# Kernel tuning notes

Measured on AMD Instinct MI355X. Metric: run time of the kernel, lower is better.

The kernel has to match this reference:

```python
import jax, jax.numpy as jnp
import numpy as np

N_HEAD = 8
D_MODEL = 512
D_K = 64
D_V = 64
LN_EPS = 1e-6


def setup_inputs() -> dict:
    key = jax.random.key(0)
    ks = jax.random.split(key, 8)
    B, L = 4, 1024
    inp = {
        "q": jax.random.normal(ks[0], (B, L, D_MODEL), dtype=jnp.float32),
        "k": jax.random.normal(ks[1], (B, L, D_MODEL), dtype=jnp.float32),
        "v": jax.random.normal(ks[2], (B, L, D_MODEL), dtype=jnp.float32),
        "w_qs": jax.random.normal(ks[3], (D_MODEL, N_HEAD * D_K), dtype=jnp.float32) * 0.02,
        "w_ks": jax.random.normal(ks[4], (D_MODEL, N_HEAD * D_K), dtype=jnp.float32) * 0.02,
        "w_vs": jax.random.normal(ks[5], (D_MODEL, N_HEAD * D_V), dtype=jnp.float32) * 0.02,
        "w_sk": jax.random.normal(ks[6], (D_V, N_HEAD * D_V), dtype=jnp.float32) * 0.02,
        "w_fc": jax.random.normal(ks[7], (D_V, D_MODEL), dtype=jnp.float32) * 0.02,
        "ln_gamma": jnp.ones((D_MODEL,), dtype=jnp.float32),
        "ln_beta": jnp.zeros((D_MODEL,), dtype=jnp.float32),
    }
    return inp


def reference(q, k, v, w_qs, w_ks, w_vs, w_sk, w_fc, ln_gamma, ln_beta):
    B, Lq, _ = q.shape
    Lk = k.shape[1]
    temp = jnp.asarray(D_K ** 0.5, q.dtype)
    residual = q

    # QKV projections (bias=False), split heads: [B, H, L, d]
    qh = (q @ w_qs).reshape(B, Lq, N_HEAD, D_K).transpose(0, 2, 1, 3)
    kh = (k @ w_ks).reshape(B, Lk, N_HEAD, D_K).transpose(0, 2, 1, 3)
    vh = (v @ w_vs).reshape(B, Lk, N_HEAD, D_V).transpose(0, 2, 1, 3)

    # scaled dot-product attention (dropout in eval mode = identity)
    attn = jax.nn.softmax(jnp.einsum('bhqd,bhkd->bhqk', qh / temp, kh), axis=-1)
    o = jnp.einsum('bhqk,bhkd->bhqd', attn, vh)  # [B, H, Lq, D_V]

    # SPA: selective parallel attention head gating
    u = o.sum(axis=1)                       # [B, Lq, D_V]
    s = u.mean(axis=1)                      # adaptive avg pool over Lq -> [B, D_V]
    g = jax.nn.softmax((s @ w_sk).reshape(B, N_HEAD, D_V), axis=1)  # softmax over heads
    f = o * g[:, :, None, :]                # gate each head, broadcast over Lq
    qo = f.sum(axis=1)                      # sum heads -> [B, Lq, D_V]

    # fc + residual + LayerNorm (dropout eval = identity)
    out = qo @ w_fc + residual              # [B, Lq, D_MODEL]
    mu = out.mean(axis=-1, keepdims=True)
    var = out.var(axis=-1, keepdims=True)
    out = (out - mu) * jax.lax.rsqrt(var + LN_EPS) * ln_gamma + ln_beta
    return out, attn
```

## Files before the change

### kernel.cpp

```cpp
#include <hip/hip_runtime.h>
#include <hip/hip_bf16.h>
#include <cstdint>

#define NH 8
#define DM 512
#define DH 64
#define NB 4
#define SL 1024

typedef __attribute__((ext_vector_type(8))) short bf16x8;
typedef __attribute__((ext_vector_type(4))) float f32x4;

static __device__ __forceinline__ float bf2f(short s) {
  union { unsigned int u; float f; } c;
  c.u = ((unsigned int)(unsigned short)s) << 16;
  return c.f;
}
static __device__ __forceinline__ unsigned short f2bfbits(float f) {
  union { float f; unsigned int u; } c; c.f = f;
  unsigned int lsb = (c.u >> 16) & 1u;
  unsigned int r = c.u + 0x7fffu + lsb;
  return (unsigned short)(r >> 16);
}

__global__ __launch_bounds__(256) void k_cvt_act(
    const float* __restrict__ q, const float* __restrict__ k, const float* __restrict__ v,
    ushort* __restrict__ qb, ushort* __restrict__ kb, ushort* __restrict__ vb) {
  int i = blockIdx.x * 256 + threadIdx.x;
  {
    float4 f = ((const float4*)q)[i];
    ushort4 r = { f2bfbits(f.x), f2bfbits(f.y), f2bfbits(f.z), f2bfbits(f.w) };
    *(ushort4*)(qb + 4 * i) = r;
  }
  {
    float4 f = ((const float4*)k)[i];
    ushort4 r = { f2bfbits(f.x), f2bfbits(f.y), f2bfbits(f.z), f2bfbits(f.w) };
    *(ushort4*)(kb + 4 * i) = r;
  }
  {
    float4 f = ((const float4*)v)[i];
    ushort4 r = { f2bfbits(f.x), f2bfbits(f.y), f2bfbits(f.z), f2bfbits(f.w) };
    *(ushort4*)(vb + 4 * i) = r;
  }
}

__global__ __launch_bounds__(256) void k_cvt_wT(
    const float* __restrict__ w0, const float* __restrict__ w1, const float* __restrict__ w2,
    ushort* __restrict__ o0, ushort* __restrict__ o1, ushort* __restrict__ o2) {
  __shared__ ushort tile[64][65];
  const float* src = blockIdx.z == 0 ? w0 : (blockIdx.z == 1 ? w1 : w2);
  ushort* dst = blockIdx.z == 0 ? o0 : (blockIdx.z == 1 ? o1 : o2);
  int k0 = blockIdx.x * 64, n0 = blockIdx.y * 64;
  int t = threadIdx.x;
  #pragma unroll
  for (int i = 0; i < 16; ++i) {
    int lin = t + i * 256, r = lin >> 6, c = lin & 63;
    tile[r][c] = f2bfbits(src[(size_t)(k0 + r) * DM + n0 + c]);
  }
  __syncthreads();
  #pragma unroll
  for (int i = 0; i < 16; ++i) {
    int lin = t + i * 256, r = lin >> 6, c = lin & 63;
    dst[(size_t)(n0 + r) * DM + k0 + c] = tile[c][r];
  }
}

__global__ __launch_bounds__(256) void k_cvt_wfc(const float* __restrict__ w, ushort* __restrict__ o) {
  int i = blockIdx.x * 256 + threadIdx.x;
  float4 f = ((const float4*)w)[i];
  ushort4 r = { f2bfbits(f.x), f2bfbits(f.y), f2bfbits(f.z), f2bfbits(f.w) };
  *(ushort4*)(o + 4 * i) = r;
}

__global__ __launch_bounds__(256) void k_proj(
    const ushort* __restrict__ qb, const ushort* __restrict__ kb, const ushort* __restrict__ vb,
    const ushort* __restrict__ wqT, const ushort* __restrict__ wkT, const ushort* __restrict__ wvT,
    ushort* __restrict__ Qh, ushort* __restrict__ Kh, ushort* __restrict__ VhT) {
  int z = blockIdx.z;
  const ushort* A = z == 0 ? qb : (z == 1 ? kb : vb);
  const ushort* W = z == 0 ? wqT : (z == 1 ? wkT : wvT);
  ushort* Out = z == 0 ? Qh : (z == 1 ? Kh : VhT);
  float scale = z == 0 ? 0.125f : 1.0f;

  int wid = threadIdx.x >> 6, l = threadIdx.x & 63;
  int lr = l & 15, lg = l >> 4;
  int row0 = blockIdx.x * 64 + wid * 16;
  int col0 = blockIdx.y * 64;
  const ushort* Arow = A + (size_t)(row0 + lr) * DM + lg * 8;

  f32x4 acc0 = {0.f, 0.f, 0.f, 0.f}, acc1 = acc0, acc2 = acc0, acc3 = acc0;
  #pragma unroll 4
  for (int kt = 0; kt < 16; ++kt) {
    bf16x8 a = *(const bf16x8*)(Arow + kt * 32);
    bf16x8 b0 = *(const bf16x8*)(W + (size_t)(col0 + 0 * 16 + lr) * DM + kt * 32 + lg * 8);
    bf16x8 b1 = *(const bf16x8*)(W + (size_t)(col0 + 1 * 16 + lr) * DM + kt * 32 + lg * 8);
    bf16x8 b2 = *(const bf16x8*)(W + (size_t)(col0 + 2 * 16 + lr) * DM + kt * 32 + lg * 8);
    bf16x8 b3 = *(const bf16x8*)(W + (size_t)(col0 + 3 * 16 + lr) * DM + kt * 32 + lg * 8);
    acc0 = __builtin_amdgcn_mfma_f32_16x16x32_bf16(a, b0, acc0, 0, 0, 0);
    acc1 = __builtin_amdgcn_mfma_f32_16x16x32_bf16(a, b1, acc1, 0, 0, 0);
    acc2 = __builtin_amdgcn_mfma_f32_16x16x32_bf16(a, b2, acc2, 0, 0, 0);
    acc3 = __builtin_amdgcn_mfma_f32_16x16x32_bf16(a, b3, acc3, 0, 0, 0);
  }
  f32x4 accs[4] = {acc0, acc1, acc2, acc3};
  #pragma unroll
  for (int ct = 0; ct < 4; ++ct) {
    int gcol = col0 + ct * 16 + lr;
    int h = gcol >> 6, d = gcol & 63;
    #pragma unroll
    for (int r = 0; r < 4; ++r) {
      int grow = row0 + lg * 4 + r;
      int bb = grow >> 10, li = grow & 1023;
      float val = accs[ct][r] * scale;
      size_t addr;
      if (z == 2) addr = ((size_t)((bb * NH + h) * DH + d)) * SL + li;
      else        addr = ((size_t)((bb * NH + h) * SL + li)) * DH + d;
      Out[addr] = f2bfbits(val);
    }
  }
}

__global__ __launch_bounds__(256, 4) void k_attn(
    const ushort* __restrict__ Qh, const ushort* __restrict__ Kh, const ushort* __restrict__ VhT,
    float* __restrict__ attn_out, float* __restrict__ O) {
  __shared__ __align__(16) ushort Sl[16 * 1024];
  __shared__ float wmax[4][16];

  int rt = blockIdx.x, h = blockIdx.y, bb = blockIdx.z;
  int bh = bb * NH + h;
  int wid = threadIdx.x >> 6, l = threadIdx.x & 63;
  int lr = l & 15, lg = l >> 4;
  char* Sb = (char*)Sl;

  const ushort* Qbase = Qh + ((size_t)(bh * SL + rt * 16 + lr)) * DH + lg * 8;
  bf16x8 aQ0 = *(const bf16x8*)(Qbase);
  bf16x8 aQ1 = *(const bf16x8*)(Qbase + 32);
  const ushort* Kbase = Kh + (size_t)bh * SL * DH;

  float mloc[4] = {-1e30f, -1e30f, -1e30f, -1e30f};
  #pragma unroll 4
  for (int ct = 0; ct < 16; ++ct) {
    int col0 = wid * 256 + ct * 16;
    const ushort* kp = Kbase + (size_t)(col0 + lr) * DH + lg * 8;
    bf16x8 b0 = *(const bf16x8*)(kp);
    bf16x8 b1 = *(const bf16x8*)(kp + 32);
    f32x4 acc = {0.f, 0.f, 0.f, 0.f};
    acc = __builtin_amdgcn_mfma_f32_16x16x32_bf16(aQ0, b0, acc, 0, 0, 0);
    acc = __builtin_amdgcn_mfma_f32_16x16x32_bf16(aQ1, b1, acc, 0, 0, 0);
    #pragma unroll
    for (int r = 0; r < 4; ++r) {
      int row = lg * 4 + r;
      ushort us = f2bfbits(acc[r]);
      *(ushort*)(Sb + (((row << 11) + ((col0 + lr) << 1)) ^ ((row & 7) << 4))) = us;
      mloc[r] = fmaxf(mloc[r], bf2f(us));
    }
  }
  #pragma unroll
  for (int r = 0; r < 4; ++r) {
    float m = mloc[r];
    m = fmaxf(m, __shfl_xor(m, 1));
    m = fmaxf(m, __shfl_xor(m, 2));
    m = fmaxf(m, __shfl_xor(m, 4));
    m = fmaxf(m, __shfl_xor(m, 8));
    if (lr == 0) wmax[wid][lg * 4 + r] = m;
  }
  __syncthreads();

  size_t attn_base = ((size_t)(bh * SL + rt * 16)) * SL;
  #pragma unroll
  for (int rr = 0; rr < 4; ++rr) {
    int r = wid * 4 + rr;
    float M = fmaxf(fmaxf(wmax[0][r], wmax[1][r]), fmaxf(wmax[2][r], wmax[3][r]));
    float e[16];
    float s = 0.f;
    #pragma unroll
    for (int i = 0; i < 16; ++i) {
      float v = bf2f(*(ushort*)(Sb + (((r << 11) + ((l + 64 * i) << 1)) ^ ((r & 7) << 4))));
      e[i] = __expf(v - M); s += e[i];
    }
    #pragma unroll
    for (int o = 32; o; o >>= 1) s += __shfl_xor(s, o);
    float inv = 1.0f / s;
    float* arow = attn_out + attn_base + (size_t)r * SL;
    #pragma unroll
    for (int i = 0; i < 16; ++i) {
      float p = e[i] * inv;
      arow[l + 64 * i] = p;
      *(ushort*)(Sb + (((r << 11) + ((l + 64 * i) << 1)) ^ ((r & 7) << 4))) = f2bfbits(p);
    }
  }
  __syncthreads();

  const ushort* Vbase = VhT + (size_t)bh * DH * SL + (size_t)(wid * 16 + lr) * SL + lg * 8;
  f32x4 acc = {0.f, 0.f, 0.f, 0.f};
  #pragma unroll 8
  for (int kt = 0; kt < 32; ++kt) {
    bf16x8 aP = *(const bf16x8*)(Sb + (((lr << 11) + ((kt * 32 + lg * 8) << 1)) ^ ((lr & 7) << 4)));
    bf16x8 bV = *(const bf16x8*)(Vbase + kt * 32);
    acc = __builtin_amdgcn_mfma_f32_16x16x32_bf16(aP, bV, acc, 0, 0, 0);
  }
  #pragma unroll
  for (int r = 0; r < 4; ++r)
    O[((size_t)(bh * SL + rt * 16 + lg * 4 + r)) * DH + wid * 16 + lr] = acc[r];
}

__global__ __launch_bounds__(256) void k_reduce(const float* __restrict__ O, float* __restrict__ partial) {
  int slab = blockIdx.x, bb = blockIdx.y;
  int d = threadIdx.x & 63, sub = threadIdx.x >> 6;
  float s = 0.f;
  for (int h = 0; h < NH; ++h) {
    const float* base = O + ((size_t)((bb * NH + h) * SL + slab * 32 + sub * 8)) * DH + d;
    #pragma unroll
    for (int li = 0; li < 8; ++li) s += base[(size_t)li * DH];
  }
  __shared__ float red[4][64];
  red[sub][d] = s;
  __syncthreads();
  if (threadIdx.x < 64) {
    float t = red[0][d] + red[1][d] + red[2][d] + red[3][d];
    partial[(bb * 32 + slab) * 64 + d] = t;
  }
}

__global__ __launch_bounds__(256) void k_gate(const float* __restrict__ partial,
                                              const float* __restrict__ wsk, float* __restrict__ g) {
  int bb = blockIdx.x;
  int t = threadIdx.x;
  __shared__ float red[4][64];
  __shared__ float sl[64];
  __shared__ float logit[512];
  int d = t & 63, q4 = t >> 6;
  float s = 0.f;
  for (int i = 0; i < 8; ++i) s += partial[(bb * 32 + q4 * 8 + i) * 64 + d];
  red[q4][d] = s;
  __syncthreads();
  if (t < 64) sl[t] = (red[0][t] + red[1][t] + red[2][t] + red[3][t]) * (1.0f / 1024.0f);
  __syncthreads();
  #pragma unroll
  for (int jj = 0; jj < 2; ++jj) {
    int j = t + jj * 256;
    float lg = 0.f;
    #pragma unroll 8
    for (int c = 0; c < 64; ++c) lg += sl[c] * wsk[c * DM + j];
    logit[j] = lg;
  }
  __syncthreads();
  if (t < 64) {
    float m = -1e30f;
    #pragma unroll
    for (int h = 0; h < NH; ++h) m = fmaxf(m, logit[h * 64 + t]);
    float sum = 0.f, e[NH];
    #pragma unroll
    for (int h = 0; h < NH; ++h) { e[h] = __expf(logit[h * 64 + t] - m); sum += e[h]; }
    float inv = 1.0f / sum;
    #pragma unroll
    for (int h = 0; h < NH; ++h) g[bb * DM + h * 64 + t] = e[h] * inv;
  }
}

__global__ __launch_bounds__(256) void k_final(
    const float* __restrict__ O, const float* __restrict__ g, const ushort* __restrict__ wfc,
    const float* __restrict__ q, const float* __restrict__ gamma, const float* __restrict__ beta,
    float* __restrict__ out) {
  __shared__ __align__(16) ushort wl[32768];
  __shared__ __align__(16) float qo[16][64];
  __shared__ __align__(16) float gl[512];
  int lt = blockIdx.x, bb = blockIdx.y;
  int t = threadIdx.x;

  gl[t] = g[bb * DM + t];
  gl[t + 256] = g[bb * DM + 256 + t];
  {
    int jg2 = t & 15, hi = t >> 4;
    #pragma unroll
    for (int m = 0; m < 16; ++m) {
      int di = m * 16 + hi;
      int d = di >> 2, i8 = di & 3;
      bf16x8 w8 = *(const bf16x8*)(wfc + d * DM + jg2 * 32 + i8 * 8);
      *(bf16x8*)(wl + (size_t)(d * 64 + i8 * 16 + jg2) * 8) = w8;
    }
  }
  __syncthreads();

  int r = t >> 4, jg = t & 15;
  int l = lt * 16 + r;
  {
    float4 acc; acc.x = acc.y = acc.z = acc.w = 0.f;
    #pragma unroll
    for (int h = 0; h < NH; ++h) {
      float4 ov = *(const float4*)(O + ((size_t)((bb * NH + h) * SL + l)) * DH + jg * 4);
      float4 gv = *(const float4*)(gl + h * 64 + jg * 4);
      acc.x += ov.x * gv.x; acc.y += ov.y * gv.y; acc.z += ov.z * gv.z; acc.w += ov.w * gv.w;
    }
    *(float4*)&qo[r][jg * 4] = acc;
  }
  __syncthreads();

  float val[32];
  const float* qrow = q + ((size_t)(bb * SL + l)) * DM + jg * 32;
  #pragma unroll
  for (int i4 = 0; i4 < 8; ++i4) *(float4*)&val[i4 * 4] = *(const float4*)(qrow + i4 * 4);

  for (int d = 0; d < 64; ++d) {
    float qd = qo[r][d];
    #pragma unroll
    for (int i8 = 0; i8 < 4; ++i8) {
      bf16x8 wv8 = *(const bf16x8*)(wl + (size_t)(d * 64 + i8 * 16 + jg) * 8);
      #pragma unroll
      for (int e = 0; e < 8; ++e) val[i8 * 8 + e] += qd * bf2f(wv8[e]);
    }
  }

  float s = 0.f, ss = 0.f;
  #pragma unroll
  for (int i = 0; i < 32; ++i) { s += val[i]; ss += val[i] * val[i]; }
  #pragma unroll
  for (int m = 1; m < 16; m <<= 1) { s += __shfl_xor(s, m, 16); ss += __shfl_xor(ss, m, 16); }
  float mu = s * (1.0f / 512.0f);
  float var = ss * (1.0f / 512.0f) - mu * mu;
  float rstd = rsqrtf(var + 1e-6f);

  float* orow = out + ((size_t)(bb * SL + l)) * DM + jg * 32;
  const float* gam = gamma + jg * 32;
  const float* bet = beta + jg * 32;
  #pragma unroll
  for (int i = 0; i < 32; ++i)
    orow[i] = (val[i] - mu) * rstd * gam[i] + bet[i];
}

extern "C" void kernel_launch(void* const* d_in, const int* in_sizes, int n_in,
                              void* d_out, int out_size, void* d_ws, size_t ws_size,
                              hipStream_t stream) {
  (void)in_sizes; (void)n_in; (void)out_size; (void)ws_size;
  const float* q     = (const float*)d_in[0];
  const float* k     = (const float*)d_in[1];
  const float* v     = (const float*)d_in[2];
  const float* w_qs  = (const float*)d_in[3];
  const float* w_ks  = (const float*)d_in[4];
  const float* w_vs  = (const float*)d_in[5];
  const float* w_sk  = (const float*)d_in[6];
  const float* w_fc  = (const float*)d_in[7];
  const float* gamma = (const float*)d_in[8];
  const float* beta  = (const float*)d_in[9];

  float* out  = (float*)d_out;
  float* attn = out + (size_t)NB * SL * DM;

  char* wsb = (char*)d_ws;
  ushort* qb   = (ushort*)(wsb + 0);
  ushort* kb   = (ushort*)(wsb + 4194304);
  ushort* vb   = (ushort*)(wsb + 8388608);
  ushort* wqT  = (ushort*)(wsb + 12582912);
  ushort* wkT  = (ushort*)(wsb + 13107200);
  ushort* wvT  = (ushort*)(wsb + 13631488);
  ushort* wfcb = (ushort*)(wsb + 14155776);
  ushort* Qh   = (ushort*)(wsb + 14221312);
  ushort* Kh   = (ushort*)(wsb + 18415616);
  ushort* VhT  = (ushort*)(wsb + 22609920);
  float*  O    = (float*)(wsb + 26804224);
  float*  part = (float*)(wsb + 35192832);
  float*  gbuf = (float*)(wsb + 35225600);

  k_cvt_act<<<dim3(2048), dim3(256), 0, stream>>>(q, k, v, qb, kb, vb);
  k_cvt_wT<<<dim3(8, 8, 3), dim3(256), 0, stream>>>(w_qs, w_ks, w_vs, wqT, wkT, wvT);
  k_cvt_wfc<<<dim3(32), dim3(256), 0, stream>>>(w_fc, wfcb);
  k_proj<<<dim3(64, 8, 3), dim3(256), 0, stream>>>(qb, kb, vb, wqT, wkT, wvT, Qh, Kh, VhT);
  k_attn<<<dim3(64, 8, 4), dim3(256), 0, stream>>>(Qh, Kh, VhT, attn, O);
  k_reduce<<<dim3(32, 4), dim3(256), 0, stream>>>(O, part);
  k_gate<<<dim3(4), dim3(256), 0, stream>>>(part, w_sk, gbuf);
  k_final<<<dim3(64, 4), dim3(256), 0, stream>>>(O, gbuf, wfcb, q, gamma, beta, out);
}
```

Baseline: 169.1 us.

## Remap attention blocks to XCDs, vectorize softmax LDS and attn stores, add MFMA priority

The attention kernel now launches a flat grid and remaps block IDs so that all query tiles of a given batch-head land on the same XCD, which should improve L2 reuse of that head's K and V. The softmax pass reads and writes LDS with 4-wide vectors and writes the fp32 attention matrix with float4 stores instead of scalar ones. It also raises wave priority around the MFMA calls. The swizzled LDS addressing must remain correct for 8-byte accesses, and the XCD mapping assumes round-robin dispatch of blocks across XCDs.

```diff
diff --git a/kernel.cpp b/kernel.cpp
--- a/kernel.cpp
+++ b/kernel.cpp
@@ -125,8 +125,12 @@
   __shared__ __align__(16) ushort Sl[16 * 1024];
   __shared__ float wmax[4][16];
 
-  int rt = blockIdx.x, h = blockIdx.y, bb = blockIdx.z;
-  int bh = bb * NH + h;
+  int bid = blockIdx.x;
+  int xcd = bid & 7;
+  int loc = bid >> 3;
+  int bh  = xcd * 4 + (loc >> 6);
+  int rt  = loc & 63;
+
   int wid = threadIdx.x >> 6, l = threadIdx.x & 63;
   int lr = l & 15, lg = l >> 4;
   char* Sb = (char*)Sl;
@@ -144,8 +148,10 @@
     bf16x8 b0 = *(const bf16x8*)(kp);
     bf16x8 b1 = *(const bf16x8*)(kp + 32);
     f32x4 acc = {0.f, 0.f, 0.f, 0.f};
+    __builtin_amdgcn_s_setprio(1);
     acc = __builtin_amdgcn_mfma_f32_16x16x32_bf16(aQ0, b0, acc, 0, 0, 0);
     acc = __builtin_amdgcn_mfma_f32_16x16x32_bf16(aQ1, b1, acc, 0, 0, 0);
+    __builtin_amdgcn_s_setprio(0);
     #pragma unroll
     for (int r = 0; r < 4; ++r) {
       int row = lg * 4 + r;
@@ -173,19 +179,29 @@
     float e[16];
     float s = 0.f;
     #pragma unroll
-    for (int i = 0; i < 16; ++i) {
-      float v = bf2f(*(ushort*)(Sb + (((r << 11) + ((l + 64 * i) << 1)) ^ ((r & 7) << 4))));
-      e[i] = __expf(v - M); s += e[i];
+    for (int i = 0; i < 4; ++i) {
+      int c0 = 4 * l + 256 * i;
+      ushort4 u4 = *(const ushort4*)(Sb + (((r << 11) + (c0 << 1)) ^ ((r & 7) << 4)));
+      float v0 = bf2f(u4.x), v1 = bf2f(u4.y), v2 = bf2f(u4.z), v3 = bf2f(u4.w);
+      e[4 * i + 0] = __expf(v0 - M);
+      e[4 * i + 1] = __expf(v1 - M);
+      e[4 * i + 2] = __expf(v2 - M);
+      e[4 * i + 3] = __expf(v3 - M);
+      s += e[4 * i + 0] + e[4 * i + 1] + e[4 * i + 2] + e[4 * i + 3];
     }
     #pragma unroll
     for (int o = 32; o; o >>= 1) s += __shfl_xor(s, o);
     float inv = 1.0f / s;
     float* arow = attn_out + attn_base + (size_t)r * SL;
     #pragma unroll
-    for (int i = 0; i < 16; ++i) {
-      float p = e[i] * inv;
-      arow[l + 64 * i] = p;
-      *(ushort*)(Sb + (((r << 11) + ((l + 64 * i) << 1)) ^ ((r & 7) << 4))) = f2bfbits(p);
+    for (int i = 0; i < 4; ++i) {
+      int c0 = 4 * l + 256 * i;
+      float4 p;
+      p.x = e[4 * i + 0] * inv; p.y = e[4 * i + 1] * inv;
+      p.z = e[4 * i + 2] * inv; p.w = e[4 * i + 3] * inv;
+      *(float4*)(arow + c0) = p;
+      ushort4 pu = { f2bfbits(p.x), f2bfbits(p.y), f2bfbits(p.z), f2bfbits(p.w) };
+      *(ushort4*)(Sb + (((r << 11) + (c0 << 1)) ^ ((r & 7) << 4))) = pu;
     }
   }
   __syncthreads();
@@ -196,7 +212,9 @@
   for (int kt = 0; kt < 32; ++kt) {
     bf16x8 aP = *(const bf16x8*)(Sb + (((lr << 11) + ((kt * 32 + lg * 8) << 1)) ^ ((lr & 7) << 4)));
     bf16x8 bV = *(const bf16x8*)(Vbase + kt * 32);
+    __builtin_amdgcn_s_setprio(1);
     acc = __builtin_amdgcn_mfma_f32_16x16x32_bf16(aP, bV, acc, 0, 0, 0);
+    __builtin_amdgcn_s_setprio(0);
   }
   #pragma unroll
   for (int r = 0; r < 4; ++r)
@@ -364,7 +382,7 @@
   k_cvt_wT<<<dim3(8, 8, 3), dim3(256), 0, stream>>>(w_qs, w_ks, w_vs, wqT, wkT, wvT);
   k_cvt_wfc<<<dim3(32), dim3(256), 0, stream>>>(w_fc, wfcb);
   k_proj<<<dim3(64, 8, 3), dim3(256), 0, stream>>>(qb, kb, vb, wqT, wkT, wvT, Qh, Kh, VhT);
-  k_attn<<<dim3(64, 8, 4), dim3(256), 0, stream>>>(Qh, Kh, VhT, attn, O);
+  k_attn<<<dim3(2048), dim3(256), 0, stream>>>(Qh, Kh, VhT, attn, O);
   k_reduce<<<dim3(32, 4), dim3(256), 0, stream>>>(O, part);
   k_gate<<<dim3(4), dim3(256), 0, stream>>>(part, w_sk, gbuf);
   k_final<<<dim3(64, 4), dim3(256), 0, stream>>>(O, gbuf, wfcb, q, gamma, beta, out);
```

After: 176.1 us. +4.1%, slower.
